# Optimization experiments

Hardware: AMD Instinct MI355X
Metric: run time of the kernel (lower is better)

Reference implementation:

```python
import jax, jax.numpy as jnp
import numpy as np

B, C, DET, T = 16, 1, 512, 180  # batch, channels, detector size (= image side, circle=True), n angles


def setup_inputs() -> dict:
    key = jax.random.key(0)
    x = jax.random.normal(key, (B, C, DET, T), dtype=jnp.float32)  # sinogram [B,C,det,theta]
    return {"x": x}


def _ramp_filter(x):
    """skimage-style ramp (Ram-Lak) filter along detector axis (axis=2)."""
    det = x.shape[2]
    size = max(64, int(2 ** np.ceil(np.log2(2 * det))))  # zero-padded FFT length
    n = np.concatenate([np.arange(1, size // 2 + 1, 2), np.arange(size // 2 - 1, 0, -2)])
    f = np.zeros(size, dtype=np.float64)
    f[0] = 0.25
    f[1::2] = -1.0 / (np.pi * n) ** 2
    fourier = (2.0 * np.real(np.fft.fft(f))).astype(np.float32)  # [size]
    xp = jnp.pad(x, ((0, 0), (0, 0), (0, size - det), (0, 0)))
    proj = jnp.fft.fft(xp, axis=2) * fourier[None, None, :, None]
    return jnp.real(jnp.fft.ifft(proj, axis=2))[:, :, :det, :].astype(x.dtype)


def _forward(x):
    b, c, det, n_theta = x.shape
    xf = _ramp_filter(x)
    # align_corners=False unit grid over the image (circle=True -> grid side == det)
    u = ((2.0 * jnp.arange(det, dtype=x.dtype) + 1.0) / det - 1.0)
    yg = u[:, None]  # [det,1] (meshgrid 'ij': Y varies over rows)
    xg = u[None, :]  # [1,det]
    rad = jnp.arange(n_theta, dtype=x.dtype) * jnp.asarray(np.pi / 180.0, x.dtype)
    cos_t, sin_t = jnp.cos(rad), jnp.sin(rad)

    # Note: the grid X coord theta_x[i]=(2i+1)/T-1 maps (align_corners=False) to pixel
    # index exactly i, so the width-axis bilinear interp reduces to taking angle column i.
    def body(reco, inp):
        i, c_, s_ = inp
        col = jax.lax.dynamic_index_in_dim(xf, i, axis=3, keepdims=False)  # [B,C,det]
        t = xg * c_ - yg * s_                      # [det,det] rotated coordinate
        iy = ((t + 1.0) * det - 1.0) / 2.0         # grid_sample align_corners=False
        i0f = jnp.floor(iy)
        w1 = iy - i0f
        w0 = 1.0 - w1
        i0 = i0f.astype(jnp.int32)
        i1 = i0 + 1
        m0 = ((i0 >= 0) & (i0 < det)).astype(xf.dtype)  # zeros padding
        m1 = ((i1 >= 0) & (i1 < det)).astype(xf.dtype)
        g0 = jnp.take(col, jnp.clip(i0, 0, det - 1), axis=2)  # [B,C,det,det]
        g1 = jnp.take(col, jnp.clip(i1, 0, det - 1), axis=2)
        return reco + (w0 * m0) * g0 + (w1 * m1) * g1, None

    reco0 = jnp.zeros((b, c, det, det), xf.dtype)
    reco, _ = jax.lax.scan(body, reco0, (jnp.arange(n_theta), cos_t, sin_t))

    # reconstruction circle mask (scikit=False -> radius^2 <= 1 - 1/in_size)
    mask = (xg ** 2 + yg ** 2) <= (1.0 - 1.0 / det)
    reco = jnp.where(mask[None, None], reco, jnp.zeros((), reco.dtype))
    return reco * jnp.asarray(np.pi / (2.0 * n_theta), reco.dtype)


def reference(x):
    return _forward(x)
```

## Files before the change

### kernel.cpp

```cpp
#include <hip/hip_runtime.h>
#include <math.h>

#define DET 512
#define NB  16
#define NT  180
#define PI_D 3.14159265358979323846
#define NPAIR 89
#define PADQ 108
#define PKROW 768
#define NGRP3 30
#define NLIVE 109

#define TT_OFF   8192
#define XF0_OFF  (TT_OFF + 512*512*2)
#define XF90_OFF (XF0_OFF + 32768)
#define PK_OFF   (XF90_OFF + 32768)

typedef _Float16 half8  __attribute__((ext_vector_type(8)));
typedef _Float16 half2v __attribute__((ext_vector_type(2)));
typedef float    float4v __attribute__((ext_vector_type(4)));

__device__ inline void fmix_lo(float& acc, float w, unsigned int pk) {
  asm("v_fma_mix_f32 %0, %1, %2, %0 op_sel_hi:[0,1,0]"
      : "+v"(acc) : "v"(w), "v"(pk));
}
__device__ inline void fmix_hi(float& acc, float w, unsigned int pk) {
  asm("v_fma_mix_f32 %0, %1, %2, %0 op_sel:[0,1,0] op_sel_hi:[0,1,0]"
      : "+v"(acc) : "v"(w), "v"(pk));
}

__global__ __launch_bounds__(256) void init_kernel(char* __restrict__ wsb) {
  int tid = threadIdx.x;
  int d = blockIdx.x;
  _Float16* tth = (_Float16*)(wsb + TT_OFF);
#pragma unroll
  for (int c = 0; c < 2; c++) {
    int k = tid * 2 + c;
    int delta = d - k;
    float w;
    if (delta == 0) w = 0.5f;
    else if (delta & 1) { double dd = (double)delta; w = (float)(-2.0 / (PI_D * PI_D * dd * dd)); }
    else w = 0.f;
    tth[(size_t)d * 512 + k] = (_Float16)(w * 1024.0f);
  }
  if (d == 0 && tid < NPAIR) {
    float2* trigp = (float2*)wsb;
    int t = tid + 1, u = 179 - tid;
    float rt = (float)t * (float)(PI_D / 180.0);
    float ru = (float)u * (float)(PI_D / 180.0);
    double ct = cos((double)rt), st = sin((double)rt);
    double cu = cos((double)ru), su = sin((double)ru);
    float2 cs;
    cs.x = (float)((ct - cu) * 0.5);
    cs.y = (float)((st + su) * 0.5);
    trigp[tid] = cs;
  }
}

__global__ __launch_bounds__(256) void filter_kernel(const float* __restrict__ x,
                                                     char* __restrict__ wsb) {
  __shared__ _Float16 xs_h[16][512];
  __shared__ _Float16 xs_l[16][512];
  __shared__ float xfs[16][65];
  const _Float16* tth = (const _Float16*)(wsb + TT_OFF);
  unsigned int* pkg = (unsigned int*)(wsb + PK_OFF);

  int tid = threadIdx.x;
  int p = blockIdx.x, b = blockIdx.y;
  int dt0 = blockIdx.z * 2;

  int m = tid & 15, kp = tid >> 4;
  int tS;
  if (p < 11) tS = (m < 8) ? (8 * p + 1 + m) : (164 - 8 * p + m);
  else        tS = (m == 0) ? 89 : ((m == 1) ? 91 : ((m == 3) ? 90 : 0));
  const float* xb = x + (size_t)b * DET * NT + tS;
#pragma unroll 8
  for (int pass = 0; pass < 16; pass++) {
    int k = pass * 32 + kp * 2;
    int c = k >> 3, h = k & 7;
    int phys = (((c ^ (m & 7)) << 3) | h);
    float v0 = xb[(size_t)k * NT];
    float v1 = xb[(size_t)(k + 1) * NT];
    _Float16 h0 = (_Float16)v0, h1 = (_Float16)v1;
    half2v hh = {h0, h1};
    half2v ll = {(_Float16)(v0 - (float)h0), (_Float16)(v1 - (float)h1)};
    *(half2v*)&xs_h[m][phys] = hh;
    *(half2v*)&xs_l[m][phys] = ll;
  }
  __syncthreads();

  int nprb = (p < 11) ? 8 : 1;
  int tpb0 = (p < 11) ? 8 * p : 88;
  if (blockIdx.z == 0) {
    int idx = (tid < 108) ? tid : (620 + (tid - 108));
    for (int pr = 0; pr < nprb; pr++)
      pkg[((size_t)b * NPAIR + tpb0 + pr) * PKROW + idx] = 0u;
  }

  int lane = tid & 63, wv = tid >> 6;
  int mm = lane & 15, q = lane >> 4;
  const _Float16* arh = &xs_h[mm][0];
  const _Float16* arl = &xs_l[mm][0];
  int e = mm & 7;
  int mp = tid >> 5, cc = (tid & 31) * 2;
  int rT = (p < 11) ? mp : 0;
  int rU = (p < 11) ? (15 - mp) : 1;
  int tpp = (p < 11) ? (8 * p + mp) : 88;
  bool dopack = (p < 11) || (mp == 0);

  for (int dti = 0; dti < 2; dti++) {
    int dt = dt0 + dti;
    int dw = dt * 64 + wv * 16 + mm;
    const _Float16* th = tth + (size_t)dw * 512;
    float4v acc0 = {0.f, 0.f, 0.f, 0.f};
    float4v acc1 = {0.f, 0.f, 0.f, 0.f};
#pragma unroll 4
    for (int kc = 0; kc < 512; kc += 32) {
      int ph = ((((kc >> 3) + q) ^ e) << 3);
      half8 Ah = *(const half8*)&arh[ph];
      half8 Al = *(const half8*)&arl[ph];
      half8 Bh = *(const half8*)&th[kc + q * 8];
      acc0 = __builtin_amdgcn_mfma_f32_16x16x32_f16(Ah, Bh, acc0, 0, 0, 0);
      acc1 = __builtin_amdgcn_mfma_f32_16x16x32_f16(Al, Bh, acc1, 0, 0, 0);
    }
    if (dti > 0) __syncthreads();
#pragma unroll
    for (int i = 0; i < 4; i++)
      xfs[q * 4 + i][wv * 16 + mm] = (acc0[i] + acc1[i]) * 0.0009765625f;
    __syncthreads();
    if (dopack) {
      float ft0 = xfs[rT][cc], ft1 = xfs[rT][cc + 1];
      float fu0 = xfs[rU][cc], fu1 = xfs[rU][cc + 1];
      auto p0 = __builtin_amdgcn_cvt_pkrtz(ft0, fu0);
      auto p1 = __builtin_amdgcn_cvt_pkrtz(ft1, fu1);
      uint2 dstv;
      __builtin_memcpy(&dstv.x, &p0, 4);
      __builtin_memcpy(&dstv.y, &p1, 4);
      *(uint2*)&pkg[((size_t)b * NPAIR + tpp) * PKROW + PADQ + dt * 64 + cc] = dstv;
    }
    if (p == 11 && tid < 64) {
      float* f0  = (float*)(wsb + XF0_OFF)  + (size_t)b * DET;
      float* f90 = (float*)(wsb + XF90_OFF) + (size_t)b * DET;
      f0[dt * 64 + tid]  = xfs[2][tid];
      f90[dt * 64 + tid] = xfs[3][tid];
    }
  }
}

__global__ __launch_bounds__(256, 8) void backproj_kernel(
    const char* __restrict__ wsb, float* __restrict__ out) {
  __shared__ unsigned int pk[2][3][PKROW];
  int tid = threadIdx.x;
  int b   = blockIdx.y;
  int bx  = blockIdx.x;
  int lx = tid & 31, ly = tid >> 5;
  float* ob = out + (size_t)b * DET * DET;

  if (bx == NLIVE) {
    const int DPX[19] = {0,0,0,0,0,0,0,0, 1,1,1,1,1, 2,2,2, 3,3, 4};
    const int DPY[19] = {0,1,2,3,4,5,6,7, 0,1,2,3,4, 0,1,2, 0,1, 0};
#pragma unroll
    for (int t = 0; t < 19; t++) {
      int tx = DPX[t] * 32, ty = DPY[t] * 16;
      int X1 = tx + lx, X2 = 511 - X1;
#pragma unroll
      for (int j = 0; j < 2; j++) {
        int Y1 = ty + ly + 8 * j, Y2 = 511 - Y1;
        ob[(size_t)Y1 * DET + X1] = 0.f;
        ob[(size_t)Y1 * DET + X2] = 0.f;
        ob[(size_t)Y2 * DET + X2] = 0.f;
        ob[(size_t)Y2 * DET + X1] = 0.f;
      }
    }
    return;
  }

  int px = (bx >= 8) + (bx >= 19) + (bx >= 32) + (bx >= 46) +
           (bx >= 61) + (bx >= 77) + (bx >= 93);
  unsigned long long STARTS = 0x5D4D3D2E20130800ULL;
  unsigned long long FIRSTS = 0x0000000102030508ULL;
  int st = (int)((STARTS >> (8 * px)) & 0xFF);
  int fi = (int)((FIRSTS >> (8 * px)) & 0xFF);
  int tx = px * 32;
  int ty = (bx - st + fi) * 16;

  int X1 = tx + lx, X2 = 511 - X1;

  const float2* trigp = (const float2*)wsb;
  const unsigned int* pkg = (const unsigned int*)(wsb + PK_OFF) + (size_t)b * NPAIR * PKROW;

  int w = tid >> 6, l = tid & 63;

  float p_ = (float)(tx + lx) - 255.5f;
  float q0 = (float)(ty + ly) - 255.5f;

  int mkx = 449 - 2 * tx;
  bool live[2];
#pragma unroll
  for (int j = 0; j < 2; j++) {
    int mky = 509 - 2 * ty - 4 * w - 16 * j;
    live[j] = (mkx * mkx + mky * mky <= 261632);
  }

  float A1[2] = {0,0}, A2[2] = {0,0}, A3[2] = {0,0}, A4[2] = {0,0};

  auto stage_group = [&](int g, int par) {
    int tp = 3 * g + w;
    if (w < 3 && tp < NPAIR) {
      const unsigned int* src = pkg + (size_t)tp * PKROW + l * 4;
      char* dst = (char*)&pk[par][w][0];
#pragma unroll
      for (int c3 = 0; c3 < 3; c3++)
        __builtin_amdgcn_global_load_lds(
            (const __attribute__((address_space(1))) unsigned int*)(src + c3 * 256),
            (__attribute__((address_space(3))) unsigned int*)(dst + c3 * 1024),
            16, 0, 0);
    }
  };

  stage_group(0, 0);
  __syncthreads();

  for (int g = 0; g < NGRP3; g++) {
    if (g + 1 < NGRP3) stage_group(g + 1, (g + 1) & 1);
    int npair = (g < NGRP3 - 1) ? 3 : (NPAIR - 3 * (NGRP3 - 1));
    for (int cgi = 0; cgi < npair; cgi++) {
      int tp = 3 * g + cgi;
      float2 cs = trigp[tp];
      float c = cs.x, s = cs.y;
      const unsigned int* col = &pk[g & 1][cgi][0];
      float inner = fmaf(-s, q0, 255.5f + (float)PADQ);
      float iyA = fmaf( c, p_, inner);
      float iyB = fmaf(-c, p_, inner);
      float s8 = 8.f * s;
#pragma unroll
      for (int j = 0; j < 2; j++) {
        if (live[j]) {
          int   iA = (int)iyA;
          float wA = __builtin_amdgcn_fractf(iyA);
          int   iB = (int)iyB;
          float wB = __builtin_amdgcn_fractf(iyB);
          float vA = 1.f - wA, vB = 1.f - wB;
          uint2 dA, dB, dMA, dMB;
          __builtin_memcpy(&dA,  &col[iA], 8);
          __builtin_memcpy(&dB,  &col[iB], 8);
          __builtin_memcpy(&dMA, &col[726 - iA], 8);
          __builtin_memcpy(&dMB, &col[726 - iB], 8);
          fmix_lo(A1[j], vA, dA.x);  fmix_lo(A1[j], wA, dA.y);
          fmix_hi(A1[j], vB, dB.x);  fmix_hi(A1[j], wB, dB.y);
          fmix_lo(A2[j], vB, dB.x);  fmix_lo(A2[j], wB, dB.y);
          fmix_hi(A2[j], vA, dA.x);  fmix_hi(A2[j], wA, dA.y);
          fmix_lo(A3[j], wA, dMA.x); fmix_lo(A3[j], vA, dMA.y);
          fmix_hi(A3[j], wB, dMB.x); fmix_hi(A3[j], vB, dMB.y);
          fmix_lo(A4[j], wB, dMB.x); fmix_lo(A4[j], vB, dMB.y);
          fmix_hi(A4[j], wA, dMA.x); fmix_hi(A4[j], vA, dMA.y);
        }
        iyA -= s8; iyB -= s8;
      }
    }
    __syncthreads();
  }

  const float* f0  = (const float*)(wsb + XF0_OFF)  + (size_t)b * DET;
  const float* f90 = (const float*)(wsb + XF90_OFF) + (size_t)b * DET;
  float g0a = f0[X1], g0b = f0[X2];
  int kx = 2 * X1 - 511;
  const float SC = (float)(PI_D / 360.0);
#pragma unroll
  for (int j = 0; j < 2; j++) {
    int Y1 = ty + ly + 8 * j, Y2 = 511 - Y1;
    float g90a = f90[Y2];
    float g90b = f90[Y1];
    int ky = 2 * Y1 - 511;
    bool in = (kx * kx + ky * ky) <= 261632;
    float P1 = A1[j] + g0a + g90a;
    float P2 = A2[j] + g0b + g90a;
    float P3 = A3[j] + g0b + g90b;
    float P4 = A4[j] + g0a + g90b;
    ob[(size_t)Y1 * DET + X1] = in ? P1 * SC : 0.f;
    ob[(size_t)Y1 * DET + X2] = in ? P2 * SC : 0.f;
    ob[(size_t)Y2 * DET + X2] = in ? P3 * SC : 0.f;
    ob[(size_t)Y2 * DET + X1] = in ? P4 * SC : 0.f;
  }
}

extern "C" void kernel_launch(void* const* d_in, const int* in_sizes, int n_in,
                              void* d_out, int out_size, void* d_ws, size_t ws_size,
                              hipStream_t stream) {
  (void)in_sizes; (void)n_in; (void)out_size; (void)ws_size;
  const float* x = (const float*)d_in[0];
  float* out = (float*)d_out;
  char*  wsb = (char*)d_ws;

  init_kernel<<<512, 256, 0, stream>>>(wsb);
  filter_kernel<<<dim3(12, 16, 4), 256, 0, stream>>>(x, wsb);
  backproj_kernel<<<dim3(NLIVE + 1, 16), 256, 0, stream>>>(wsb, out);
}
```

Baseline: 164.9 us.

## Store filtered projections as fp32 pairs and backproject with packed FP32 FMAs

The packed filtered columns become fp32 (t,u) pairs instead of fp16 pairs, and the backprojection inner loop uses v_pk_fma_f32 with op_sel swizzles, so one instruction updates two accumulators instead of one v_fma_mix each. The doubled row size means LDS staging now holds 2 angle pairs per group instead of 3, giving 45 groups and more barriers, and launch bounds drop from 8 to 6 waves. This trades LDS and global traffic and occupancy for half as many FMA instructions and higher precision.

```diff
diff --git a/kernel.cpp b/kernel.cpp
--- a/kernel.cpp
+++ b/kernel.cpp
@@ -8,7 +8,7 @@
 #define NPAIR 89
 #define PADQ 108
 #define PKROW 768
-#define NGRP3 30
+#define NGRP2 45
 #define NLIVE 109
 
 #define TT_OFF   8192
@@ -19,14 +19,23 @@
 typedef _Float16 half8  __attribute__((ext_vector_type(8)));
 typedef _Float16 half2v __attribute__((ext_vector_type(2)));
 typedef float    float4v __attribute__((ext_vector_type(4)));
-
-__device__ inline void fmix_lo(float& acc, float w, unsigned int pk) {
-  asm("v_fma_mix_f32 %0, %1, %2, %0 op_sel_hi:[0,1,0]"
-      : "+v"(acc) : "v"(w), "v"(pk));
-}
-__device__ inline void fmix_hi(float& acc, float w, unsigned int pk) {
-  asm("v_fma_mix_f32 %0, %1, %2, %0 op_sel:[0,1,0] op_sel_hi:[0,1,0]"
-      : "+v"(acc) : "v"(w), "v"(pk));
+typedef float    float2v __attribute__((ext_vector_type(2)));
+
+__device__ inline void pk_l(float2v& a, float2v p, float2v d) {
+  asm("v_pk_fma_f32 %0, %1, %2, %0 op_sel:[0,0,0] op_sel_hi:[0,1,1]"
+      : "+v"(a) : "v"(p), "v"(d));
+}
+__device__ inline void pk_h(float2v& a, float2v p, float2v d) {
+  asm("v_pk_fma_f32 %0, %1, %2, %0 op_sel:[1,0,0] op_sel_hi:[1,1,1]"
+      : "+v"(a) : "v"(p), "v"(d));
+}
+__device__ inline void pk_ls(float2v& a, float2v p, float2v d) {
+  asm("v_pk_fma_f32 %0, %1, %2, %0 op_sel:[0,1,0] op_sel_hi:[0,0,1]"
+      : "+v"(a) : "v"(p), "v"(d));
+}
+__device__ inline void pk_hs(float2v& a, float2v p, float2v d) {
+  asm("v_pk_fma_f32 %0, %1, %2, %0 op_sel:[1,1,0] op_sel_hi:[1,0,1]"
+      : "+v"(a) : "v"(p), "v"(d));
 }
 
 __global__ __launch_bounds__(256) void init_kernel(char* __restrict__ wsb) {
@@ -63,7 +72,7 @@
   __shared__ _Float16 xs_l[16][512];
   __shared__ float xfs[16][65];
   const _Float16* tth = (const _Float16*)(wsb + TT_OFF);
-  unsigned int* pkg = (unsigned int*)(wsb + PK_OFF);
+  float2v* pkg = (float2v*)(wsb + PK_OFF);
 
   int tid = threadIdx.x;
   int p = blockIdx.x, b = blockIdx.y;
@@ -93,8 +102,9 @@
   int tpb0 = (p < 11) ? 8 * p : 88;
   if (blockIdx.z == 0) {
     int idx = (tid < 108) ? tid : (620 + (tid - 108));
+    float2v z = {0.f, 0.f};
     for (int pr = 0; pr < nprb; pr++)
-      pkg[((size_t)b * NPAIR + tpb0 + pr) * PKROW + idx] = 0u;
+      pkg[((size_t)b * NPAIR + tpb0 + pr) * PKROW + idx] = z;
   }
 
   int lane = tid & 63, wv = tid >> 6;
@@ -131,12 +141,11 @@
     if (dopack) {
       float ft0 = xfs[rT][cc], ft1 = xfs[rT][cc + 1];
       float fu0 = xfs[rU][cc], fu1 = xfs[rU][cc + 1];
-      auto p0 = __builtin_amdgcn_cvt_pkrtz(ft0, fu0);
-      auto p1 = __builtin_amdgcn_cvt_pkrtz(ft1, fu1);
-      uint2 dstv;
-      __builtin_memcpy(&dstv.x, &p0, 4);
-      __builtin_memcpy(&dstv.y, &p1, 4);
-      *(uint2*)&pkg[((size_t)b * NPAIR + tpp) * PKROW + PADQ + dt * 64 + cc] = dstv;
+      struct { float2v a, b; } st;
+      st.a.x = ft0; st.a.y = fu0;
+      st.b.x = ft1; st.b.y = fu1;
+      __builtin_memcpy(&pkg[((size_t)b * NPAIR + tpp) * PKROW + PADQ + dt * 64 + cc],
+                       &st, 16);
     }
     if (p == 11 && tid < 64) {
       float* f0  = (float*)(wsb + XF0_OFF)  + (size_t)b * DET;
@@ -147,9 +156,9 @@
   }
 }
 
-__global__ __launch_bounds__(256, 8) void backproj_kernel(
+__global__ __launch_bounds__(256, 6) void backproj_kernel(
     const char* __restrict__ wsb, float* __restrict__ out) {
-  __shared__ unsigned int pk[2][3][PKROW];
+  __shared__ float2v pk[2][2][PKROW];
   int tid = threadIdx.x;
   int b   = blockIdx.y;
   int bx  = blockIdx.x;
@@ -187,7 +196,7 @@
   int X1 = tx + lx, X2 = 511 - X1;
 
   const float2* trigp = (const float2*)wsb;
-  const unsigned int* pkg = (const unsigned int*)(wsb + PK_OFF) + (size_t)b * NPAIR * PKROW;
+  const char* pk2 = wsb + PK_OFF + (size_t)b * NPAIR * (PKROW * 8);
 
   int w = tid >> 6, l = tid & 63;
 
@@ -202,17 +211,19 @@
     live[j] = (mkx * mkx + mky * mky <= 261632);
   }
 
-  float A1[2] = {0,0}, A2[2] = {0,0}, A3[2] = {0,0}, A4[2] = {0,0};
+  float2v acc12[2], acc34[2];
+#pragma unroll
+  for (int j = 0; j < 2; j++) { acc12[j] = (float2v){0.f,0.f}; acc34[j] = (float2v){0.f,0.f}; }
 
   auto stage_group = [&](int g, int par) {
-    int tp = 3 * g + w;
-    if (w < 3 && tp < NPAIR) {
-      const unsigned int* src = pkg + (size_t)tp * PKROW + l * 4;
+    int tp = 2 * g + w;
+    if (w < 2 && tp < NPAIR) {
+      const char* src = pk2 + (size_t)tp * (PKROW * 8) + l * 16;
       char* dst = (char*)&pk[par][w][0];
 #pragma unroll
-      for (int c3 = 0; c3 < 3; c3++)
+      for (int c3 = 0; c3 < 6; c3++)
         __builtin_amdgcn_global_load_lds(
-            (const __attribute__((address_space(1))) unsigned int*)(src + c3 * 256),
+            (const __attribute__((address_space(1))) unsigned int*)(src + c3 * 1024),
             (__attribute__((address_space(3))) unsigned int*)(dst + c3 * 1024),
             16, 0, 0);
     }
@@ -221,14 +232,14 @@
   stage_group(0, 0);
   __syncthreads();
 
-  for (int g = 0; g < NGRP3; g++) {
-    if (g + 1 < NGRP3) stage_group(g + 1, (g + 1) & 1);
-    int npair = (g < NGRP3 - 1) ? 3 : (NPAIR - 3 * (NGRP3 - 1));
+  for (int g = 0; g < NGRP2; g++) {
+    if (g + 1 < NGRP2) stage_group(g + 1, (g + 1) & 1);
+    int npair = (g < NGRP2 - 1) ? 2 : (NPAIR - 2 * (NGRP2 - 1));
     for (int cgi = 0; cgi < npair; cgi++) {
-      int tp = 3 * g + cgi;
+      int tp = 2 * g + cgi;
       float2 cs = trigp[tp];
       float c = cs.x, s = cs.y;
-      const unsigned int* col = &pk[g & 1][cgi][0];
+      const float2v* col = &pk[g & 1][cgi][0];
       float inner = fmaf(-s, q0, 255.5f + (float)PADQ);
       float iyA = fmaf( c, p_, inner);
       float iyB = fmaf(-c, p_, inner);
@@ -240,20 +251,21 @@
           float wA = __builtin_amdgcn_fractf(iyA);
           int   iB = (int)iyB;
           float wB = __builtin_amdgcn_fractf(iyB);
-          float vA = 1.f - wA, vB = 1.f - wB;
-          uint2 dA, dB, dMA, dMB;
-          __builtin_memcpy(&dA,  &col[iA], 8);
-          __builtin_memcpy(&dB,  &col[iB], 8);
-          __builtin_memcpy(&dMA, &col[726 - iA], 8);
-          __builtin_memcpy(&dMB, &col[726 - iB], 8);
-          fmix_lo(A1[j], vA, dA.x);  fmix_lo(A1[j], wA, dA.y);
-          fmix_hi(A1[j], vB, dB.x);  fmix_hi(A1[j], wB, dB.y);
-          fmix_lo(A2[j], vB, dB.x);  fmix_lo(A2[j], wB, dB.y);
-          fmix_hi(A2[j], vA, dA.x);  fmix_hi(A2[j], wA, dA.y);
-          fmix_lo(A3[j], wA, dMA.x); fmix_lo(A3[j], vA, dMA.y);
-          fmix_hi(A3[j], wB, dMB.x); fmix_hi(A3[j], vB, dMB.y);
-          fmix_lo(A4[j], wB, dMB.x); fmix_lo(A4[j], vB, dMB.y);
-          fmix_hi(A4[j], wA, dMA.x); fmix_hi(A4[j], vA, dMA.y);
+          float2v pA; pA.x = 1.f - wA; pA.y = wA;
+          float2v pB; pB.x = 1.f - wB; pB.y = wB;
+          struct { float2v e0, e1; } qA, qB, qMA, qMB;
+          __builtin_memcpy(&qA,  &col[iA], 16);
+          __builtin_memcpy(&qB,  &col[iB], 16);
+          __builtin_memcpy(&qMA, &col[726 - iA], 16);
+          __builtin_memcpy(&qMB, &col[726 - iB], 16);
+          pk_l (acc12[j], pA, qA.e0);
+          pk_h (acc12[j], pA, qA.e1);
+          pk_ls(acc12[j], pB, qB.e0);
+          pk_hs(acc12[j], pB, qB.e1);
+          pk_h (acc34[j], pA, qMA.e0);
+          pk_l (acc34[j], pA, qMA.e1);
+          pk_hs(acc34[j], pB, qMB.e0);
+          pk_ls(acc34[j], pB, qMB.e1);
         }
         iyA -= s8; iyB -= s8;
       }
@@ -273,10 +285,10 @@
     float g90b = f90[Y1];
     int ky = 2 * Y1 - 511;
     bool in = (kx * kx + ky * ky) <= 261632;
-    float P1 = A1[j] + g0a + g90a;
-    float P2 = A2[j] + g0b + g90a;
-    float P3 = A3[j] + g0b + g90b;
-    float P4 = A4[j] + g0a + g90b;
+    float P1 = acc12[j].x + g0a + g90a;
+    float P2 = acc12[j].y + g0b + g90a;
+    float P3 = acc34[j].x + g0b + g90b;
+    float P4 = acc34[j].y + g0a + g90b;
     ob[(size_t)Y1 * DET + X1] = in ? P1 * SC : 0.f;
     ob[(size_t)Y1 * DET + X2] = in ? P2 * SC : 0.f;
     ob[(size_t)Y2 * DET + X2] = in ? P3 * SC : 0.f;
```

New measurement: 190.1 us. 1.15x slower.
